# Kernel optimization log

Measured on AMD Instinct MI355X. Metric: run time of the kernel, lower is better.

## Reference

```python
import jax, jax.numpy as jnp
import numpy as np

EPS = 1e-5

def _layernorm(h):
    # parameter-free LayerNorm over last dim (elementwise_affine=False)
    mu = jnp.mean(h, axis=-1, keepdims=True)
    var = jnp.mean(jnp.square(h - mu), axis=-1, keepdims=True)
    return (h - mu) / jnp.sqrt(var + EPS)

def setup_inputs() -> dict:
    key = jax.random.key(0)
    k1, k2, k3, k4 = jax.random.split(key, 4)
    B, D, F_, I = 16, 37, 4096, 64
    x = jax.random.normal(k1, (B, D, F_), dtype=jnp.float32)
    s = 1.0 / np.sqrt(D)  # ~ torch Linear default init scale
    Wq = jax.random.normal(k2, (D, I), dtype=jnp.float32) * s
    Wk = jax.random.normal(k3, (D, I), dtype=jnp.float32) * s
    Wv = jax.random.normal(k4, (D, I), dtype=jnp.float32) * s
    return {"x": x, "Wq": Wq, "Wk": Wk, "Wv": Wv}

def reference(x, Wq, Wk, Wv):
    # x: [B, depth, featuresize] -> entities [B, F, depth]
    xb = jnp.transpose(x, (0, 2, 1))
    q = _layernorm(jnp.einsum('bfd,di->bfi', xb, Wq))
    k = _layernorm(jnp.einsum('bfd,di->bfi', xb, Wk))
    v = _layernorm(jnp.einsum('bfd,di->bfi', xb, Wv))
    d = q.shape[-1]
    att = jnp.einsum('bqi,bki->bqk', q, k) / jnp.sqrt(jnp.float32(d))
    # faithful to torch: softmax over dim=1 (the query axis), not the key axis
    weights = jax.nn.softmax(att, axis=-2)
    return jnp.einsum('bqk,bki->bqi', weights, v)
```

## Files before the change

### kernel.cpp

```cpp
#include <hip/hip_runtime.h>
#include <math.h>

#define B_  16
#define D_  37
#define F_  4096
#define I_  64
#define EPS 1e-5f
#define QSCALE 0.18033688011112042f
#define NQS 2
#define NKS 2

typedef unsigned short u16;
typedef __bf16 bf16x8 __attribute__((ext_vector_type(8)));
typedef __bf16 bf16x2v __attribute__((ext_vector_type(2)));
typedef float  f32x16 __attribute__((ext_vector_type(16)));
typedef float  f32x2v __attribute__((ext_vector_type(2)));
typedef unsigned int u32x4 __attribute__((ext_vector_type(4)));
typedef int i32x2 __attribute__((ext_vector_type(2)));

#define ZERO16 {0,0,0,0, 0,0,0,0, 0,0,0,0, 0,0,0,0}
#define MFMA32(a, b, c) __builtin_amdgcn_mfma_f32_32x32x16_bf16((a), (b), (c), 0, 0, 0)

#if __has_builtin(__builtin_amdgcn_exp2f)
#define EX2(x) __builtin_amdgcn_exp2f(x)
#else
#define EX2(x) exp2f(x)
#endif
#if __has_builtin(__builtin_amdgcn_rcpf)
#define RCP(x) __builtin_amdgcn_rcpf(x)
#else
#define RCP(x) (1.f / (x))
#endif

__device__ __forceinline__ u16 f2b(float f) {
  unsigned u = __builtin_bit_cast(unsigned, f);
  return (u16)((u + 0x7fffu + ((u >> 16) & 1u)) >> 16);
}
__device__ __forceinline__ float b2f(u16 h) {
  return __builtin_bit_cast(float, (unsigned)h << 16);
}
__device__ __forceinline__ unsigned pk2(float lo, float hi) {
  f32x2v f = {lo, hi};
  bf16x2v h = __builtin_convertvector(f, bf16x2v);
  return __builtin_bit_cast(unsigned, h);
}

__device__ __forceinline__ void plswap(unsigned& a, unsigned& b) {
#if __has_builtin(__builtin_amdgcn_permlane32_swap)
  i32x2 r = __builtin_amdgcn_permlane32_swap((int)a, (int)b, false, false);
  a = (unsigned)r[0];
  b = (unsigned)r[1];
#else
  const int lh = (int)((threadIdx.x & 63) >> 5);
  unsigned pa = (unsigned)__shfl_xor((int)a, 32, 64);
  unsigned pb = (unsigned)__shfl_xor((int)b, 32, 64);
  unsigned na = lh ? pb : a;
  unsigned nb = lh ? b : pa;
  a = na;
  b = nb;
#endif
}

__device__ __forceinline__ void build_af(const f32x16& s, bf16x8& f0, bf16x8& f1) {
  float e[16];
#pragma unroll
  for (int r = 0; r < 16; ++r) e[r] = EX2(s[r]);
  unsigned a = pk2(e[0], e[1]),   bq = pk2(e[2], e[3]);
  unsigned c = pk2(e[4], e[5]),   d  = pk2(e[6], e[7]);
  plswap(a, c);
  plswap(bq, d);
  u32x4 v0 = {a, bq, c, d};
  f0 = __builtin_bit_cast(bf16x8, v0);
  unsigned ee = pk2(e[8], e[9]),  ff = pk2(e[10], e[11]);
  unsigned g  = pk2(e[12], e[13]), h = pk2(e[14], e[15]);
  plswap(ee, g);
  plswap(ff, h);
  u32x4 v1 = {ee, ff, g, h};
  f1 = __builtin_bit_cast(bf16x8, v1);
}

__device__ __forceinline__ bf16x8 ldfrag(const u16* base, int row, int kb) {
  return *(const bf16x8*)(base + (row << 6) + ((kb ^ (row & 7)) << 3));
}
__device__ __forceinline__ int soff_l(int c) {
  const int r = c >> 3, cb = c & 7;
  return (r << 6) + ((cb ^ (r & 7)) << 3);
}
__device__ __forceinline__ int soff_g(int c, int spitch) {
  return (c >> 3) * spitch + ((c & 7) << 3);
}

__device__ __forceinline__ int swz512(int wg) {
  return (wg & 7) * 64 + (wg >> 3);
}

__global__ __launch_bounds__(256) void qkv_ln_k(
    const float* __restrict__ x,
    const float* __restrict__ Wq, const float* __restrict__ Wk,
    const float* __restrict__ Wv,
    u16* __restrict__ qn, u16* __restrict__ kn, u16* __restrict__ vt) {
  __shared__ float sW[3 * D_ * I_];
  __shared__ float xs[D_ * 64];
  __shared__ __align__(16) u16 vtile[64 * 72];

  const int t = threadIdx.x;
  const int b = blockIdx.y;
  const int f0 = blockIdx.x * 64;

  for (int i = t; i < D_ * I_; i += 256) {
    sW[i]               = Wq[i];
    sW[D_ * I_ + i]     = Wk[i];
    sW[2 * D_ * I_ + i] = Wv[i];
  }
  const float* xb = x + (size_t)b * D_ * F_ + f0;
  for (int i = t; i < D_ * 64; i += 256)
    xs[i] = xb[(size_t)(i >> 6) * F_ + (i & 63)];
  __syncthreads();

  const int lane = t & 63, w = t >> 6;

  for (int it = 0; it < 16; ++it) {
    const int fl = w * 16 + it;
    float hq = 0.f, hk = 0.f, hv = 0.f;
#pragma unroll
    for (int d = 0; d < D_; ++d) {
      const float xv = xs[d * 64 + fl];
      hq = fmaf(xv, sW[d * 64 + lane], hq);
      hk = fmaf(xv, sW[D_ * I_ + d * 64 + lane], hk);
      hv = fmaf(xv, sW[2 * D_ * I_ + d * 64 + lane], hv);
    }
    auto lnorm = [&](float a) -> float {
      float s = a;
#pragma unroll
      for (int o = 32; o > 0; o >>= 1) s += __shfl_xor(s, o, 64);
      const float mu = s * (1.f / 64.f);
      const float d0 = a - mu;
      float v = d0 * d0;
#pragma unroll
      for (int o = 32; o > 0; o >>= 1) v += __shfl_xor(v, o, 64);
      return d0 * rsqrtf(v * (1.f / 64.f) + EPS);
    };
    const size_t fo = ((size_t)b * F_ + f0 + fl) * I_ + lane;
    qn[fo] = f2b(lnorm(hq) * QSCALE);
    kn[fo] = f2b(lnorm(hk));
    vtile[lane * 72 + fl] = f2b(lnorm(hv));
  }
  __syncthreads();
  for (int p = 0; p < 2; ++p) {
    const int c = p * 256 + t;
    const int r = c >> 3, off = (c & 7) * 8;
    const int4 v = *(const int4*)&vtile[r * 72 + off];
    *(int4*)(vt + ((size_t)b * I_ + r) * F_ + f0 + off) = v;
  }
}

__global__ __launch_bounds__(256, 2) void attn_stats_k(
    const u16* __restrict__ qn, const u16* __restrict__ kn,
    float* __restrict__ zp) {
  __shared__ __align__(16) u16 sm[16384];

  const int t = threadIdx.x, lane = t & 63, w = t >> 6;
  const int l31 = lane & 31, lh = lane >> 5;
  const int lg = swz512((int)blockIdx.x);
  const int k0 = (lg & 15) * 256, b = (lg >> 4) & 15, qh = lg >> 8;

  const u16* kp = kn + ((size_t)b * F_ + k0 + w * 64 + l31) * I_ + lh * 8;
  bf16x8 kf[2][4];
#pragma unroll
  for (int kb2 = 0; kb2 < 2; ++kb2)
#pragma unroll
    for (int ic = 0; ic < 4; ++ic)
      kf[kb2][ic] = *(const bf16x8*)(kp + kb2 * 32 * I_ + ic * 16);

  int qoff_l[2], qoff_g[2];
#pragma unroll
  for (int p = 0; p < 2; ++p) {
    const int c = p * 256 + t;
    qoff_l[p] = soff_l(c);
    qoff_g[p] = soff_g(c, 64);
  }

  const u16* qsrc = qn + ((size_t)b * F_ + qh * (F_ / NQS)) * I_;
#pragma unroll
  for (int s = 0; s < 2; ++s)
#pragma unroll
    for (int p = 0; p < 2; ++p)
      *(int4*)(sm + s * 4096 + qoff_l[p]) =
          *(const int4*)(qsrc + s * 64 * I_ + qoff_g[p]);
  qsrc += 128 * I_;

  float Zc[2][2] = {{0.f, 0.f}, {0.f, 0.f}};

  auto qcompute = [&](const u16* Qc) {
    f32x16 a00 = ZERO16, a01 = ZERO16, a10 = ZERO16, a11 = ZERO16;
    __builtin_amdgcn_s_setprio(1);
#pragma unroll
    for (int ic = 0; ic < 4; ++ic) {
      const bf16x8 q0f = ldfrag(Qc, l31, ic * 2 + lh);
      const bf16x8 q1f = ldfrag(Qc + 32 * 64, l31, ic * 2 + lh);
      a00 = MFMA32(q0f, kf[0][ic], a00);
      a01 = MFMA32(q0f, kf[1][ic], a01);
      a10 = MFMA32(q1f, kf[0][ic], a10);
      a11 = MFMA32(q1f, kf[1][ic], a11);
    }
    __builtin_amdgcn_s_setprio(0);
#pragma unroll
    for (int r = 0; r < 16; ++r) {
      Zc[0][0] += EX2(a00[r]);
      Zc[0][1] += EX2(a01[r]);
      Zc[1][0] += EX2(a10[r]);
      Zc[1][1] += EX2(a11[r]);
    }
  };

  const int NC = F_ / NQS / 128;

  for (int c = 0; c < NC; ++c) {
    const int cur = (c & 1) * 8192;
    const int nxt = cur ^ 8192;
    const bool pf = (c + 1 < NC);
    __syncthreads();
    int4 qr0, qr1;
    if (pf) {
      qr0 = *(const int4*)(qsrc + qoff_g[0]);
      qr1 = *(const int4*)(qsrc + qoff_g[1]);
    }
    qcompute(sm + cur);
    if (pf) {
      *(int4*)(sm + nxt + qoff_l[0]) = qr0;
      *(int4*)(sm + nxt + qoff_l[1]) = qr1;
      qr0 = *(const int4*)(qsrc + 64 * I_ + qoff_g[0]);
      qr1 = *(const int4*)(qsrc + 64 * I_ + qoff_g[1]);
    }
    qcompute(sm + cur + 4096);
    if (pf) {
      *(int4*)(sm + nxt + 4096 + qoff_l[0]) = qr0;
      *(int4*)(sm + nxt + 4096 + qoff_l[1]) = qr1;
      qsrc += 128 * I_;
    }
  }

#pragma unroll
  for (int kb2 = 0; kb2 < 2; ++kb2) {
    float Zt = Zc[0][kb2] + Zc[1][kb2];
    Zt += __shfl_xor(Zt, 32, 64);
    if (lane < 32)
      zp[((size_t)qh * B_ + b) * F_ + k0 + w * 64 + kb2 * 32 + lane] = Zt;
  }
}

__global__ __launch_bounds__(256) void vscale_k(u16* __restrict__ vt,
                                                const float* __restrict__ zp) {
  const int b = blockIdx.y;
  const int off = (blockIdx.x * 256 + (int)threadIdx.x) * 8;
  const int k = off & (F_ - 1);
  const size_t BF = (size_t)B_ * F_;
  u16* p = vt + (size_t)b * I_ * F_ + off;
  const float* z = zp + (size_t)b * F_ + k;
  int4 raw = *(const int4*)p;
  u16 es[8], os[8];
  *(int4*)es = raw;
#pragma unroll
  for (int j = 0; j < 8; ++j) {
    const float v = b2f(es[j]);
    float zs = 0.f;
#pragma unroll
    for (int qh = 0; qh < NQS; ++qh) zs += z[qh * BF + j];
    os[j] = f2b(v * RCP(zs));
  }
  *(int4*)p = *(int4*)os;
}

__global__ __launch_bounds__(256, 2) void attn_out_k(
    const u16* __restrict__ qn, const u16* __restrict__ kn,
    const u16* __restrict__ vt, float* __restrict__ out,
    u16* __restrict__ pout) {
  __shared__ __align__(16) u16 sm[32768];

  const int t = threadIdx.x, lane = t & 63, w = t >> 6;
  const int l31 = lane & 31, lh = lane >> 5;
  const int lg = swz512((int)blockIdx.x);
  const int q0 = (lg & 15) * 256, b = (lg >> 4) & 15, ks = lg >> 8;

  const u16* qp = qn + ((size_t)b * F_ + q0 + w * 64 + l31) * I_ + lh * 8;
  bf16x8 qf[2][4];
#pragma unroll
  for (int qb2 = 0; qb2 < 2; ++qb2)
#pragma unroll
    for (int ic = 0; ic < 4; ++ic)
      qf[qb2][ic] = *(const bf16x8*)(qp + qb2 * 32 * I_ + ic * 16);

  int off_l[2], kg[2], vg[2];
#pragma unroll
  for (int p = 0; p < 2; ++p) {
    const int c = p * 256 + t;
    off_l[p] = soff_l(c);
    kg[p] = soff_g(c, 64);
    vg[p] = soff_g(c, F_);
  }

  const u16* ksrc = kn + ((size_t)b * F_ + ks * (F_ / NKS)) * I_;
  const u16* vsrc = vt + (size_t)b * I_ * F_ + ks * (F_ / NKS);
#pragma unroll
  for (int s = 0; s < 2; ++s)
#pragma unroll
    for (int p = 0; p < 2; ++p) {
      *(int4*)(sm + s * 4096 + off_l[p]) =
          *(const int4*)(ksrc + s * 64 * I_ + kg[p]);
      *(int4*)(sm + 16384 + s * 4096 + off_l[p]) =
          *(const int4*)(vsrc + s * 64 + vg[p]);
    }
  ksrc += 128 * I_;
  vsrc += 128;

  f32x16 o00 = ZERO16, o01 = ZERO16, o10 = ZERO16, o11 = ZERO16;

  auto compute64 = [&](const u16* Kc, const u16* Vc) {
    f32x16 s00 = ZERO16, s01 = ZERO16, s10 = ZERO16, s11 = ZERO16;
    __builtin_amdgcn_s_setprio(1);
#pragma unroll
    for (int ic = 0; ic < 4; ++ic) {
      const bf16x8 ak0 = ldfrag(Kc, l31, ic * 2 + lh);
      const bf16x8 ak1 = ldfrag(Kc + 32 * 64, l31, ic * 2 + lh);
      s00 = MFMA32(ak0, qf[0][ic], s00);
      s01 = MFMA32(ak0, qf[1][ic], s01);
      s10 = MFMA32(ak1, qf[0][ic], s10);
      s11 = MFMA32(ak1, qf[1][ic], s11);
    }
    __builtin_amdgcn_s_setprio(0);

    bf16x8 af[2][4];
    build_af(s00, af[0][0], af[0][1]);
    build_af(s10, af[0][2], af[0][3]);
    build_af(s01, af[1][0], af[1][1]);
    build_af(s11, af[1][2], af[1][3]);

    __builtin_amdgcn_s_setprio(1);
#pragma unroll
    for (int kb4 = 0; kb4 < 4; ++kb4) {
      const bf16x8 bv0 = ldfrag(Vc, l31, kb4 * 2 + lh);
      const bf16x8 bv1 = ldfrag(Vc + 32 * 64, l31, kb4 * 2 + lh);
      o00 = MFMA32(af[0][kb4], bv0, o00);
      o01 = MFMA32(af[0][kb4], bv1, o01);
      o10 = MFMA32(af[1][kb4], bv0, o10);
      o11 = MFMA32(af[1][kb4], bv1, o11);
    }
    __builtin_amdgcn_s_setprio(0);
  };

  const int NC = F_ / NKS / 128;

  for (int c = 0; c < NC; ++c) {
    const int cur = (c & 1) * 8192;
    const int nxt = cur ^ 8192;
    const bool pf = (c + 1 < NC);
    __syncthreads();
    int4 kr0, kr1, vr0, vr1;
    if (pf) {
      kr0 = *(const int4*)(ksrc + kg[0]);
      kr1 = *(const int4*)(ksrc + kg[1]);
      vr0 = *(const int4*)(vsrc + vg[0]);
      vr1 = *(const int4*)(vsrc + vg[1]);
    }
    compute64(sm + cur, sm + 16384 + cur);
    if (pf) {
      *(int4*)(sm + nxt + off_l[0])         = kr0;
      *(int4*)(sm + nxt + off_l[1])         = kr1;
      *(int4*)(sm + 16384 + nxt + off_l[0]) = vr0;
      *(int4*)(sm + 16384 + nxt + off_l[1]) = vr1;
      kr0 = *(const int4*)(ksrc + 64 * I_ + kg[0]);
      kr1 = *(const int4*)(ksrc + 64 * I_ + kg[1]);
      vr0 = *(const int4*)(vsrc + 64 + vg[0]);
      vr1 = *(const int4*)(vsrc + 64 + vg[1]);
    }
    compute64(sm + cur + 4096, sm + 16384 + cur + 4096);
    if (pf) {
      *(int4*)(sm + nxt + 4096 + off_l[0])         = kr0;
      *(int4*)(sm + nxt + 4096 + off_l[1])         = kr1;
      *(int4*)(sm + 16384 + nxt + 4096 + off_l[0]) = vr0;
      *(int4*)(sm + 16384 + nxt + 4096 + off_l[1]) = vr1;
      ksrc += 128 * I_;
      vsrc += 128;
    }
  }

  if (ks == 0) {
    float* ob = out + ((size_t)b * F_ + q0 + w * 64) * I_;
#pragma unroll
    for (int r = 0; r < 16; ++r) {
      const int qr = (r & 3) + 8 * (r >> 2) + 4 * lh;
      ob[(size_t)qr * I_ + l31]              = o00[r];
      ob[(size_t)qr * I_ + 32 + l31]         = o01[r];
      ob[(size_t)(32 + qr) * I_ + l31]       = o10[r];
      ob[(size_t)(32 + qr) * I_ + 32 + l31]  = o11[r];
    }
  } else {
    u16* pb = pout + ((size_t)b * F_ + q0 + w * 64) * I_;
#pragma unroll
    for (int r = 0; r < 16; ++r) {
      const int qr = (r & 3) + 8 * (r >> 2) + 4 * lh;
      pb[(size_t)qr * I_ + l31]              = f2b(o00[r]);
      pb[(size_t)qr * I_ + 32 + l31]         = f2b(o01[r]);
      pb[(size_t)(32 + qr) * I_ + l31]       = f2b(o10[r]);
      pb[(size_t)(32 + qr) * I_ + 32 + l31]  = f2b(o11[r]);
    }
  }
}

__global__ __launch_bounds__(256) void reduce_k(float* __restrict__ out,
                                                const u16* __restrict__ pout) {
  const size_t i = ((size_t)blockIdx.x * 256 + threadIdx.x) * 8;
  float4 a0 = *(const float4*)(out + i);
  float4 a1 = *(const float4*)(out + i + 4);
  int4 praw = *(const int4*)(pout + i);
  u16 es[8];
  *(int4*)es = praw;
  a0.x += b2f(es[0]); a0.y += b2f(es[1]); a0.z += b2f(es[2]); a0.w += b2f(es[3]);
  a1.x += b2f(es[4]); a1.y += b2f(es[5]); a1.z += b2f(es[6]); a1.w += b2f(es[7]);
  *(float4*)(out + i)     = a0;
  *(float4*)(out + i + 4) = a1;
}

extern "C" void kernel_launch(void* const* d_in, const int* in_sizes, int n_in,
                              void* d_out, int out_size, void* d_ws,
                              size_t ws_size, hipStream_t stream) {
  const float* x  = (const float*)d_in[0];
  const float* Wq = (const float*)d_in[1];
  const float* Wk = (const float*)d_in[2];
  const float* Wv = (const float*)d_in[3];
  float* out = (float*)d_out;

  const size_t NBF = (size_t)B_ * F_ * I_;
  u16* qn   = (u16*)d_ws;
  u16* kn   = qn + NBF;
  u16* vt   = kn + NBF;
  float* zp = (float*)(vt + NBF);
  u16* pout = (u16*)(zp + (size_t)NQS * B_ * F_);

  qkv_ln_k<<<dim3(F_ / 64, B_), 256, 0, stream>>>(x, Wq, Wk, Wv, qn, kn, vt);
  attn_stats_k<<<dim3(512), 256, 0, stream>>>(qn, kn, zp);
  vscale_k<<<dim3(I_ * F_ / 2048, B_), 256, 0, stream>>>(vt, zp);
  attn_out_k<<<dim3(512), 256, 0, stream>>>(qn, kn, vt, out, pout);
  reduce_k<<<dim3((int)(NBF / 2048)), 256, 0, stream>>>(out, pout);
}
```

Baseline: 232.9 us.

## Split key range across waves within block and reduce partials in LDS

Each block now covers 128 queries; two waves take each key half, and each wave pair shares its query tile. Partial outputs are summed in shared memory, which removes the bf16 partial buffer and the separate reduce kernel launch. Per block, the K/V tiles loaded per step double because both key halves are staged at once, while each query tile is reused across fewer waves. This also removes the bf16 rounding of the second partial, and it adds an LDS reduction step at the end of the kernel.

Result: no change. 237.2 us (+1.9%).

```diff
diff --git a/kernel.cpp b/kernel.cpp
--- a/kernel.cpp
+++ b/kernel.cpp
@@ -8,7 +8,6 @@
 #define EPS 1e-5f
 #define QSCALE 0.18033688011112042f
 #define NQS 2
-#define NKS 2
 
 typedef unsigned short u16;
 typedef __bf16 bf16x8 __attribute__((ext_vector_type(8)));
@@ -273,16 +272,16 @@
 
 __global__ __launch_bounds__(256, 2) void attn_out_k(
     const u16* __restrict__ qn, const u16* __restrict__ kn,
-    const u16* __restrict__ vt, float* __restrict__ out,
-    u16* __restrict__ pout) {
+    const u16* __restrict__ vt, float* __restrict__ out) {
   __shared__ __align__(16) u16 sm[32768];
 
   const int t = threadIdx.x, lane = t & 63, w = t >> 6;
   const int l31 = lane & 31, lh = lane >> 5;
   const int lg = swz512((int)blockIdx.x);
-  const int q0 = (lg & 15) * 256, b = (lg >> 4) & 15, ks = lg >> 8;
-
-  const u16* qp = qn + ((size_t)b * F_ + q0 + w * 64 + l31) * I_ + lh * 8;
+  const int q0 = (lg & 31) * 128, b = lg >> 5;
+  const int qb = w >> 1, kh = w & 1;
+
+  const u16* qp = qn + ((size_t)b * F_ + q0 + qb * 64 + l31) * I_ + lh * 8;
   bf16x8 qf[2][4];
 #pragma unroll
   for (int qb2 = 0; qb2 < 2; ++qb2)
@@ -299,93 +298,118 @@
     vg[p] = soff_g(c, F_);
   }
 
-  const u16* ksrc = kn + ((size_t)b * F_ + ks * (F_ / NKS)) * I_;
-  const u16* vsrc = vt + (size_t)b * I_ * F_ + ks * (F_ / NKS);
-#pragma unroll
-  for (int s = 0; s < 2; ++s)
-#pragma unroll
-    for (int p = 0; p < 2; ++p) {
-      *(int4*)(sm + s * 4096 + off_l[p]) =
-          *(const int4*)(ksrc + s * 64 * I_ + kg[p]);
-      *(int4*)(sm + 16384 + s * 4096 + off_l[p]) =
-          *(const int4*)(vsrc + s * 64 + vg[p]);
-    }
-  ksrc += 128 * I_;
-  vsrc += 128;
+  const u16* ks0 = kn + ((size_t)b * F_) * I_;
+  const u16* ks1 = kn + ((size_t)b * F_ + F_ / 2) * I_;
+  const u16* vs0 = vt + (size_t)b * I_ * F_;
+  const u16* vs1 = vs0 + F_ / 2;
+
+#pragma unroll
+  for (int p = 0; p < 2; ++p) {
+    *(int4*)(sm + off_l[p])                = *(const int4*)(ks0 + kg[p]);
+    *(int4*)(sm + 4096 + off_l[p])         = *(const int4*)(vs0 + vg[p]);
+    *(int4*)(sm + 16384 + off_l[p])        = *(const int4*)(ks1 + kg[p]);
+    *(int4*)(sm + 16384 + 4096 + off_l[p]) = *(const int4*)(vs1 + vg[p]);
+  }
+  ks0 += 64 * I_; ks1 += 64 * I_;
+  vs0 += 64;      vs1 += 64;
 
   f32x16 o00 = ZERO16, o01 = ZERO16, o10 = ZERO16, o11 = ZERO16;
-
-  auto compute64 = [&](const u16* Kc, const u16* Vc) {
-    f32x16 s00 = ZERO16, s01 = ZERO16, s10 = ZERO16, s11 = ZERO16;
-    __builtin_amdgcn_s_setprio(1);
-#pragma unroll
-    for (int ic = 0; ic < 4; ++ic) {
-      const bf16x8 ak0 = ldfrag(Kc, l31, ic * 2 + lh);
-      const bf16x8 ak1 = ldfrag(Kc + 32 * 64, l31, ic * 2 + lh);
-      s00 = MFMA32(ak0, qf[0][ic], s00);
-      s01 = MFMA32(ak0, qf[1][ic], s01);
-      s10 = MFMA32(ak1, qf[0][ic], s10);
-      s11 = MFMA32(ak1, qf[1][ic], s11);
-    }
-    __builtin_amdgcn_s_setprio(0);
-
-    bf16x8 af[2][4];
-    build_af(s00, af[0][0], af[0][1]);
-    build_af(s10, af[0][2], af[0][3]);
-    build_af(s01, af[1][0], af[1][1]);
-    build_af(s11, af[1][2], af[1][3]);
-
-    __builtin_amdgcn_s_setprio(1);
-#pragma unroll
-    for (int kb4 = 0; kb4 < 4; ++kb4) {
-      const bf16x8 bv0 = ldfrag(Vc, l31, kb4 * 2 + lh);
-      const bf16x8 bv1 = ldfrag(Vc + 32 * 64, l31, kb4 * 2 + lh);
-      o00 = MFMA32(af[0][kb4], bv0, o00);
-      o01 = MFMA32(af[0][kb4], bv1, o01);
-      o10 = MFMA32(af[1][kb4], bv0, o10);
-      o11 = MFMA32(af[1][kb4], bv1, o11);
-    }
-    __builtin_amdgcn_s_setprio(0);
-  };
-
-  const int NC = F_ / NKS / 128;
+  const int sbase = kh * 16384;
+  const int NC = F_ / 2 / 64;
 
   for (int c = 0; c < NC; ++c) {
-    const int cur = (c & 1) * 8192;
-    const int nxt = cur ^ 8192;
+    const int buf = (c & 1) * 8192;
     const bool pf = (c + 1 < NC);
     __syncthreads();
-    int4 kr0, kr1, vr0, vr1;
+    int4 ka0, ka1, va0, va1, kb0, kb1, vb0, vb1;
     if (pf) {
-      kr0 = *(const int4*)(ksrc + kg[0]);
-      kr1 = *(const int4*)(ksrc + kg[1]);
-      vr0 = *(const int4*)(vsrc + vg[0]);
-      vr1 = *(const int4*)(vsrc + vg[1]);
-    }
-    compute64(sm + cur, sm + 16384 + cur);
+      ka0 = *(const int4*)(ks0 + kg[0]);
+      ka1 = *(const int4*)(ks0 + kg[1]);
+      va0 = *(const int4*)(vs0 + vg[0]);
+      va1 = *(const int4*)(vs0 + vg[1]);
+      kb0 = *(const int4*)(ks1 + kg[0]);
+      kb1 = *(const int4*)(ks1 + kg[1]);
+      vb0 = *(const int4*)(vs1 + vg[0]);
+      vb1 = *(const int4*)(vs1 + vg[1]);
+      ks0 += 64 * I_; ks1 += 64 * I_;
+      vs0 += 64;      vs1 += 64;
+    }
+
+    {
+      const u16* Kc = sm + sbase + buf;
+      const u16* Vc = Kc + 4096;
+      f32x16 s00 = ZERO16, s01 = ZERO16, s10 = ZERO16, s11 = ZERO16;
+      __builtin_amdgcn_s_setprio(1);
+#pragma unroll
+      for (int ic = 0; ic < 4; ++ic) {
+        const bf16x8 ak0 = ldfrag(Kc, l31, ic * 2 + lh);
+        const bf16x8 ak1 = ldfrag(Kc + 32 * 64, l31, ic * 2 + lh);
+        s00 = MFMA32(ak0, qf[0][ic], s00);
+        s01 = MFMA32(ak0, qf[1][ic], s01);
+        s10 = MFMA32(ak1, qf[0][ic], s10);
+        s11 = MFMA32(ak1, qf[1][ic], s11);
+      }
+      __builtin_amdgcn_s_setprio(0);
+
+      bf16x8 af[2][4];
+      build_af(s00, af[0][0], af[0][1]);
+      build_af(s10, af[0][2], af[0][3]);
+      build_af(s01, af[1][0], af[1][1]);
+      build_af(s11, af[1][2], af[1][3]);
+
+      __builtin_amdgcn_s_setprio(1);
+#pragma unroll
+      for (int kb4 = 0; kb4 < 4; ++kb4) {
+        const bf16x8 bv0 = ldfrag(Vc, l31, kb4 * 2 + lh);
+        const bf16x8 bv1 = ldfrag(Vc + 32 * 64, l31, kb4 * 2 + lh);
+        o00 = MFMA32(af[0][kb4], bv0, o00);
+        o01 = MFMA32(af[0][kb4], bv1, o01);
+        o10 = MFMA32(af[1][kb4], bv0, o10);
+        o11 = MFMA32(af[1][kb4], bv1, o11);
+      }
+      __builtin_amdgcn_s_setprio(0);
+    }
+
     if (pf) {
-      *(int4*)(sm + nxt + off_l[0])         = kr0;
-      *(int4*)(sm + nxt + off_l[1])         = kr1;
-      *(int4*)(sm + 16384 + nxt + off_l[0]) = vr0;
-      *(int4*)(sm + 16384 + nxt + off_l[1]) = vr1;
-      kr0 = *(const int4*)(ksrc + 64 * I_ + kg[0]);
-      kr1 = *(const int4*)(ksrc + 64 * I_ + kg[1]);
-      vr0 = *(const int4*)(vsrc + 64 + vg[0]);
-      vr1 = *(const int4*)(vsrc + 64 + vg[1]);
-    }
-    compute64(sm + cur + 4096, sm + 16384 + cur + 4096);
-    if (pf) {
-      *(int4*)(sm + nxt + 4096 + off_l[0])         = kr0;
-      *(int4*)(sm + nxt + 4096 + off_l[1])         = kr1;
-      *(int4*)(sm + 16384 + nxt + 4096 + off_l[0]) = vr0;
-      *(int4*)(sm + 16384 + nxt + 4096 + off_l[1]) = vr1;
-      ksrc += 128 * I_;
-      vsrc += 128;
-    }
-  }
-
-  if (ks == 0) {
-    float* ob = out + ((size_t)b * F_ + q0 + w * 64) * I_;
+      const int nxt = buf ^ 8192;
+      *(int4*)(sm + nxt + off_l[0])                = ka0;
+      *(int4*)(sm + nxt + off_l[1])                = ka1;
+      *(int4*)(sm + nxt + 4096 + off_l[0])         = va0;
+      *(int4*)(sm + nxt + 4096 + off_l[1])         = va1;
+      *(int4*)(sm + 16384 + nxt + off_l[0])        = kb0;
+      *(int4*)(sm + 16384 + nxt + off_l[1])        = kb1;
+      *(int4*)(sm + 16384 + nxt + 4096 + off_l[0]) = vb0;
+      *(int4*)(sm + 16384 + nxt + 4096 + off_l[1]) = vb1;
+    }
+  }
+
+  __syncthreads();
+  float* red = (float*)sm;
+  if (kh == 1) {
+#pragma unroll
+    for (int rq = 0; rq < 4; ++rq) {
+      float* rp = red + qb * 4096 + rq * 256 + lane * 4;
+      *(float4*)(rp)        = make_float4(o00[rq*4], o00[rq*4+1], o00[rq*4+2], o00[rq*4+3]);
+      *(float4*)(rp + 1024) = make_float4(o01[rq*4], o01[rq*4+1], o01[rq*4+2], o01[rq*4+3]);
+      *(float4*)(rp + 2048) = make_float4(o10[rq*4], o10[rq*4+1], o10[rq*4+2], o10[rq*4+3]);
+      *(float4*)(rp + 3072) = make_float4(o11[rq*4], o11[rq*4+1], o11[rq*4+2], o11[rq*4+3]);
+    }
+  }
+  __syncthreads();
+  if (kh == 0) {
+#pragma unroll
+    for (int rq = 0; rq < 4; ++rq) {
+      const float* rp = red + qb * 4096 + rq * 256 + lane * 4;
+      const float4 p0 = *(const float4*)(rp);
+      const float4 p1 = *(const float4*)(rp + 1024);
+      const float4 p2 = *(const float4*)(rp + 2048);
+      const float4 p3 = *(const float4*)(rp + 3072);
+      o00[rq*4] += p0.x; o00[rq*4+1] += p0.y; o00[rq*4+2] += p0.z; o00[rq*4+3] += p0.w;
+      o01[rq*4] += p1.x; o01[rq*4+1] += p1.y; o01[rq*4+2] += p1.z; o01[rq*4+3] += p1.w;
+      o10[rq*4] += p2.x; o10[rq*4+1] += p2.y; o10[rq*4+2] += p2.z; o10[rq*4+3] += p2.w;
+      o11[rq*4] += p3.x; o11[rq*4+1] += p3.y; o11[rq*4+2] += p3.z; o11[rq*4+3] += p3.w;
+    }
+    float* ob = out + ((size_t)b * F_ + q0 + qb * 64) * I_;
 #pragma unroll
     for (int r = 0; r < 16; ++r) {
       const int qr = (r & 3) + 8 * (r >> 2) + 4 * lh;
@@ -394,31 +418,7 @@
       ob[(size_t)(32 + qr) * I_ + l31]       = o10[r];
       ob[(size_t)(32 + qr) * I_ + 32 + l31]  = o11[r];
     }
-  } else {
-    u16* pb = pout + ((size_t)b * F_ + q0 + w * 64) * I_;
-#pragma unroll
-    for (int r = 0; r < 16; ++r) {
-      const int qr = (r & 3) + 8 * (r >> 2) + 4 * lh;
-      pb[(size_t)qr * I_ + l31]              = f2b(o00[r]);
-      pb[(size_t)qr * I_ + 32 + l31]         = f2b(o01[r]);
-      pb[(size_t)(32 + qr) * I_ + l31]       = f2b(o10[r]);
-      pb[(size_t)(32 + qr) * I_ + 32 + l31]  = f2b(o11[r]);
-    }
-  }
-}
-
-__global__ __launch_bounds__(256) void reduce_k(float* __restrict__ out,
-                                                const u16* __restrict__ pout) {
-  const size_t i = ((size_t)blockIdx.x * 256 + threadIdx.x) * 8;
-  float4 a0 = *(const float4*)(out + i);
-  float4 a1 = *(const float4*)(out + i + 4);
-  int4 praw = *(const int4*)(pout + i);
-  u16 es[8];
-  *(int4*)es = praw;
-  a0.x += b2f(es[0]); a0.y += b2f(es[1]); a0.z += b2f(es[2]); a0.w += b2f(es[3]);
-  a1.x += b2f(es[4]); a1.y += b2f(es[5]); a1.z += b2f(es[6]); a1.w += b2f(es[7]);
-  *(float4*)(out + i)     = a0;
-  *(float4*)(out + i + 4) = a1;
+  }
 }
 
 extern "C" void kernel_launch(void* const* d_in, const int* in_sizes, int n_in,
@@ -435,11 +435,9 @@
   u16* kn   = qn + NBF;
   u16* vt   = kn + NBF;
   float* zp = (float*)(vt + NBF);
-  u16* pout = (u16*)(zp + (size_t)NQS * B_ * F_);
 
   qkv_ln_k<<<dim3(F_ / 64, B_), 256, 0, stream>>>(x, Wq, Wk, Wv, qn, kn, vt);
   attn_stats_k<<<dim3(512), 256, 0, stream>>>(qn, kn, zp);
   vscale_k<<<dim3(I_ * F_ / 2048, B_), 256, 0, stream>>>(vt, zp);
-  attn_out_k<<<dim3(512), 256, 0, stream>>>(qn, kn, vt, out, pout);
-  reduce_k<<<dim3((int)(NBF / 2048)), 256, 0, stream>>>(out, pout);
-}
+  attn_out_k<<<dim3(512), 256, 0, stream>>>(qn, kn, vt, out);
+}
```

## Software-pipeline MFMA groups with exp/softmax work across half-tiles

Applied to the files above, without the earlier changes.

Splits each 64-key chunk's QK MFMA work into 32-row groups and interleaves the exp2/bf16 packing of one group with the MFMAs of the next, in both the column-sum kernel and the attention kernel. The aim is to overlap transcendental/VALU work with matrix-core work so MFMA pipes stay busy. The cost is more live accumulator registers (two pending groups), which may raise VGPR pressure and lower occupancy.

After: 233.4 us. About the same (+0.2%).

```diff
diff --git a/kernel.cpp b/kernel.cpp
--- a/kernel.cpp
+++ b/kernel.cpp
@@ -191,25 +191,21 @@
 
   float Zc[2][2] = {{0.f, 0.f}, {0.f, 0.f}};
 
-  auto qcompute = [&](const u16* Qc) {
-    f32x16 a00 = ZERO16, a01 = ZERO16, a10 = ZERO16, a11 = ZERO16;
+  auto Mg = [&](const u16* Qc, int qb, f32x16& t0, f32x16& t1) {
     __builtin_amdgcn_s_setprio(1);
 #pragma unroll
     for (int ic = 0; ic < 4; ++ic) {
-      const bf16x8 q0f = ldfrag(Qc, l31, ic * 2 + lh);
-      const bf16x8 q1f = ldfrag(Qc + 32 * 64, l31, ic * 2 + lh);
-      a00 = MFMA32(q0f, kf[0][ic], a00);
-      a01 = MFMA32(q0f, kf[1][ic], a01);
-      a10 = MFMA32(q1f, kf[0][ic], a10);
-      a11 = MFMA32(q1f, kf[1][ic], a11);
+      const bf16x8 qv = ldfrag(Qc + qb * 32 * 64, l31, ic * 2 + lh);
+      t0 = MFMA32(qv, kf[0][ic], t0);
+      t1 = MFMA32(qv, kf[1][ic], t1);
     }
     __builtin_amdgcn_s_setprio(0);
+  };
+  auto Eg = [&](int qb, const f32x16& t0, const f32x16& t1) {
 #pragma unroll
     for (int r = 0; r < 16; ++r) {
-      Zc[0][0] += EX2(a00[r]);
-      Zc[0][1] += EX2(a01[r]);
-      Zc[1][0] += EX2(a10[r]);
-      Zc[1][1] += EX2(a11[r]);
+      Zc[qb][0] += EX2(t0[r]);
+      Zc[qb][1] += EX2(t1[r]);
     }
   };
 
@@ -225,19 +221,33 @@
       qr0 = *(const int4*)(qsrc + qoff_g[0]);
       qr1 = *(const int4*)(qsrc + qoff_g[1]);
     }
-    qcompute(sm + cur);
+
+    f32x16 sA0 = ZERO16, sA1 = ZERO16;
+    Mg(sm + cur, 0, sA0, sA1);
+    f32x16 sB0 = ZERO16, sB1 = ZERO16;
+    Mg(sm + cur, 1, sB0, sB1);
+    Eg(0, sA0, sA1);
+
     if (pf) {
       *(int4*)(sm + nxt + qoff_l[0]) = qr0;
       *(int4*)(sm + nxt + qoff_l[1]) = qr1;
       qr0 = *(const int4*)(qsrc + 64 * I_ + qoff_g[0]);
       qr1 = *(const int4*)(qsrc + 64 * I_ + qoff_g[1]);
     }
-    qcompute(sm + cur + 4096);
+
+    f32x16 sC0 = ZERO16, sC1 = ZERO16;
+    Mg(sm + cur + 4096, 0, sC0, sC1);
+    Eg(1, sB0, sB1);
+    f32x16 sD0 = ZERO16, sD1 = ZERO16;
+    Mg(sm + cur + 4096, 1, sD0, sD1);
+    Eg(0, sC0, sC1);
+
     if (pf) {
       *(int4*)(sm + nxt + 4096 + qoff_l[0]) = qr0;
       *(int4*)(sm + nxt + 4096 + qoff_l[1]) = qr1;
       qsrc += 128 * I_;
     }
+    Eg(1, sD0, sD1);
   }
 
 #pragma unroll
@@ -315,35 +325,38 @@
 
   f32x16 o00 = ZERO16, o01 = ZERO16, o10 = ZERO16, o11 = ZERO16;
 
-  auto compute64 = [&](const u16* Kc, const u16* Vc) {
-    f32x16 s00 = ZERO16, s01 = ZERO16, s10 = ZERO16, s11 = ZERO16;
+  auto Sg = [&](const u16* Kc, f32x16& t0, f32x16& t1) {
     __builtin_amdgcn_s_setprio(1);
 #pragma unroll
     for (int ic = 0; ic < 4; ++ic) {
-      const bf16x8 ak0 = ldfrag(Kc, l31, ic * 2 + lh);
-      const bf16x8 ak1 = ldfrag(Kc + 32 * 64, l31, ic * 2 + lh);
-      s00 = MFMA32(ak0, qf[0][ic], s00);
-      s01 = MFMA32(ak0, qf[1][ic], s01);
-      s10 = MFMA32(ak1, qf[0][ic], s10);
-      s11 = MFMA32(ak1, qf[1][ic], s11);
+      const bf16x8 ak = ldfrag(Kc, l31, ic * 2 + lh);
+      t0 = MFMA32(ak, qf[0][ic], t0);
+      t1 = MFMA32(ak, qf[1][ic], t1);
     }
     __builtin_amdgcn_s_setprio(0);
-
-    bf16x8 af[2][4];
-    build_af(s00, af[0][0], af[0][1]);
-    build_af(s10, af[0][2], af[0][3]);
-    build_af(s01, af[1][0], af[1][1]);
-    build_af(s11, af[1][2], af[1][3]);
-
+  };
+  auto EPg = [&](const u16* Vc, int kh, const f32x16& t0, const f32x16& t1) {
+    bf16x8 a0, a1, b0, b1;
+    build_af(t0, a0, a1);
+    build_af(t1, b0, b1);
     __builtin_amdgcn_s_setprio(1);
-#pragma unroll
-    for (int kb4 = 0; kb4 < 4; ++kb4) {
+    {
+      const int kb4 = kh * 2;
       const bf16x8 bv0 = ldfrag(Vc, l31, kb4 * 2 + lh);
       const bf16x8 bv1 = ldfrag(Vc + 32 * 64, l31, kb4 * 2 + lh);
-      o00 = MFMA32(af[0][kb4], bv0, o00);
-      o01 = MFMA32(af[0][kb4], bv1, o01);
-      o10 = MFMA32(af[1][kb4], bv0, o10);
-      o11 = MFMA32(af[1][kb4], bv1, o11);
+      o00 = MFMA32(a0, bv0, o00);
+      o01 = MFMA32(a0, bv1, o01);
+      o10 = MFMA32(b0, bv0, o10);
+      o11 = MFMA32(b0, bv1, o11);
+    }
+    {
+      const int kb4 = kh * 2 + 1;
+      const bf16x8 bv0 = ldfrag(Vc, l31, kb4 * 2 + lh);
+      const bf16x8 bv1 = ldfrag(Vc + 32 * 64, l31, kb4 * 2 + lh);
+      o00 = MFMA32(a1, bv0, o00);
+      o01 = MFMA32(a1, bv1, o01);
+      o10 = MFMA32(b1, bv0, o10);
+      o11 = MFMA32(b1, bv1, o11);
     }
     __builtin_amdgcn_s_setprio(0);
   };
@@ -362,7 +375,18 @@
       vr0 = *(const int4*)(vsrc + vg[0]);
       vr1 = *(const int4*)(vsrc + vg[1]);
     }
-    compute64(sm + cur, sm + 16384 + cur);
+
+    const u16* K0 = sm + cur;
+    const u16* V0 = sm + 16384 + cur;
+    const u16* K1 = K0 + 4096;
+    const u16* V1 = V0 + 4096;
+
+    f32x16 sA0 = ZERO16, sA1 = ZERO16;
+    Sg(K0, sA0, sA1);
+    f32x16 sB0 = ZERO16, sB1 = ZERO16;
+    Sg(K0 + 32 * 64, sB0, sB1);
+    EPg(V0, 0, sA0, sA1);
+
     if (pf) {
       *(int4*)(sm + nxt + off_l[0])         = kr0;
       *(int4*)(sm + nxt + off_l[1])         = kr1;
@@ -373,7 +397,14 @@
       vr0 = *(const int4*)(vsrc + 64 + vg[0]);
       vr1 = *(const int4*)(vsrc + 64 + vg[1]);
     }
-    compute64(sm + cur + 4096, sm + 16384 + cur + 4096);
+
+    f32x16 sC0 = ZERO16, sC1 = ZERO16;
+    Sg(K1, sC0, sC1);
+    EPg(V0, 1, sB0, sB1);
+    f32x16 sD0 = ZERO16, sD1 = ZERO16;
+    Sg(K1 + 32 * 64, sD0, sD1);
+    EPg(V1, 0, sC0, sC1);
+
     if (pf) {
       *(int4*)(sm + nxt + 4096 + off_l[0])         = kr0;
       *(int4*)(sm + nxt + 4096 + off_l[1])         = kr1;
@@ -382,6 +413,7 @@
       ksrc += 128 * I_;
       vsrc += 128;
     }
+    EPg(V1, 1, sD0, sD1);
   }
 
   if (ks == 0) {
```
